# Kernel optimization log

Hardware: AMD Instinct MI355X
Metric: run time of the kernel (lower is better)

The kernel has to match this reference:

```python
import jax, jax.numpy as jnp
import numpy as np

B, T, S, M = 512, 256, 32, 4  # groups, timesteps, state dim, measure dim


def setup_inputs() -> dict:
    key = jax.random.key(0)
    k = jax.random.split(key, 7)
    obs = jax.random.normal(k[0], (B, T, M), jnp.float32)
    # stable transition matrix: scaled orthogonal
    A = jax.random.normal(k[1], (S, S), jnp.float32)
    F = (0.95 * jnp.linalg.qr(A)[0]).astype(jnp.float32)
    # PSD process noise
    Aq = jax.random.normal(k[2], (S, S), jnp.float32)
    Q = (0.05 * (Aq @ Aq.T) / S + 0.01 * jnp.eye(S)).astype(jnp.float32)
    H = (jax.random.normal(k[3], (M, S), jnp.float32) / jnp.sqrt(S)).astype(jnp.float32)
    # PSD measurement noise
    Ar = jax.random.normal(k[4], (M, M), jnp.float32)
    R = ((Ar @ Ar.T) / M + 0.1 * jnp.eye(M)).astype(jnp.float32)
    init_mean = jax.random.normal(k[5], (B, S), jnp.float32)
    Ai = jax.random.normal(k[6], (B, S, S), jnp.float32)
    init_cov = (jnp.einsum('bij,bkj->bik', Ai, Ai) / S + 0.1 * jnp.eye(S)).astype(jnp.float32)
    return {'input': obs, 'F': F, 'Q': Q, 'H': H, 'R': R,
            'init_mean': init_mean, 'init_cov': init_cov}


def reference(input, F, Q, H, R, init_mean, init_cov):
    """One-step-ahead Kalman filter predictions.
    Returns (meas_means [T,B,M], meas_covs [T,B,M,M])."""

    def step(carry, y):
        m, P = carry  # m: [B,S], P: [B,S,S]
        # --- update with observation y (time t-1) ---
        PHt = jnp.einsum('bij,mj->bim', P, H)                    # [B,S,M]
        Smeas = jnp.einsum('ms,bsn->bmn', H, PHt) + R            # [B,M,M]
        # K = P H^T S^{-1}  (S symmetric)
        K = jnp.swapaxes(jnp.linalg.solve(Smeas, jnp.swapaxes(PHt, -1, -2)), -1, -2)  # [B,S,M]
        resid = y - m @ H.T                                      # [B,M]
        m_u = m + jnp.einsum('bsm,bm->bs', K, resid)
        # (I - K H) P ; note H P = PHt^T since P symmetric
        P_u = P - jnp.einsum('bsm,bim->bsi', K, PHt)
        # --- predict ---
        m_p = m_u @ F.T
        P_p = jnp.einsum('ij,bjk,lk->bil', F, P_u, F) + Q
        # --- measurement distribution ---
        mm = m_p @ H.T                                           # [B,M]
        mc = jnp.einsum('ms,bsi,ni->bmn', H, P_p, H) + R         # [B,M,M]
        return (m_p, P_p), (mm, mc)

    # t = 0: measurement of the initial state prediction
    mm0 = init_mean @ H.T
    mc0 = jnp.einsum('ms,bsi,ni->bmn', H, init_cov, H) + R
    obs_tm1 = jnp.swapaxes(input[:, :-1, :], 0, 1)               # [T-1,B,M]
    _, (mms, mcs) = jax.lax.scan(step, (init_mean, init_cov), obs_tm1)
    meas_means = jnp.concatenate([mm0[None], mms], axis=0)       # [T,B,M]
    meas_covs = jnp.concatenate([mc0[None], mcs], axis=0)        # [T,B,M,M]
    return meas_means, meas_covs
```

## Files before the change

kernel.cpp:

```cpp
#include <hip/hip_runtime.h>

#define BB 512
#define TT 256

typedef __attribute__((ext_vector_type(8)))  short bf8;
typedef __attribute__((ext_vector_type(4)))  short bf4;
typedef __attribute__((ext_vector_type(16))) float f16v;
typedef __attribute__((ext_vector_type(4)))  float f4v;

#define MFMA(a,b,c) __builtin_amdgcn_mfma_f32_32x32x16_bf16((a),(b),(c),0,0,0)

static __device__ __forceinline__ unsigned short f2bf_rne(float x) {
    unsigned u = __builtin_bit_cast(unsigned, x);
    return (unsigned short)((u + 0x7FFFu + ((u >> 16) & 1u)) >> 16);
}
static __device__ __forceinline__ float bf2f(unsigned short h) {
    unsigned u = ((unsigned)h) << 16;
    return __builtin_bit_cast(float, u);
}
static __device__ __forceinline__ void tsplit(float x, short& hi, short& lo) {
    unsigned u = __builtin_bit_cast(unsigned, x);
    hi = (short)(u >> 16);
    float hf = __builtin_bit_cast(float, u & 0xFFFF0000u);
    float l  = x - hf;
    lo = (short)(__builtin_bit_cast(unsigned, l) >> 16);
}
static __device__ __forceinline__ bf8 ld8(const unsigned short* p) {
    bf4 a = *(const bf4*)p;
    bf4 b = *(const bf4*)(p + 4);
    bf8 r;
    r[0]=a[0]; r[1]=a[1]; r[2]=a[2]; r[3]=a[3];
    r[4]=b[0]; r[5]=b[1]; r[6]=b[2]; r[7]=b[3];
    return r;
}

__global__ __launch_bounds__(64)
void kalman_v5(const float* __restrict__ obs,
               const float* __restrict__ Fg,
               const float* __restrict__ Qg,
               const float* __restrict__ Hg,
               const float* __restrict__ Rg,
               const float* __restrict__ im,
               const float* __restrict__ ic,
               float* __restrict__ out)
{
    __shared__ __align__(16) unsigned short sT1h[32*36], sT1l[32*36];
    __shared__ __align__(16) unsigned short sPNh[4*36],  sPNl[4*36];
    __shared__ __align__(16) float sFH[36*40];
    __shared__ __align__(16) float sm[32];
    __shared__ __align__(16) float sS[16];
    __shared__ __align__(16) float sRes4[4];

    const int lane = threadIdx.x;
    const int b    = blockIdx.x;
    const int c    = lane & 31;
    const int h    = lane >> 5;

    bf8 Fh[2], Fl[2], Hh[2], Hl[2];
    #pragma unroll
    for (int kk = 0; kk < 2; ++kk) {
        #pragma unroll
        for (int j = 0; j < 8; ++j) {
            int k = kk*16 + h*8 + j;
            float f = Fg[c*32 + k];
            unsigned short fh = f2bf_rne(f);
            Fh[kk][j] = (short)fh;
            Fl[kk][j] = (short)f2bf_rne(f - bf2f(fh));
            float hv = (c < 4) ? Hg[c*32 + k] : 0.f;
            unsigned short hh = f2bf_rne(hv);
            Hh[kk][j] = (short)hh;
            Hl[kk][j] = (short)f2bf_rne(hv - bf2f(hh));
        }
    }

    f16v Qc, P;
    #pragma unroll
    for (int reg = 0; reg < 16; ++reg) {
        int row = (reg & 3) + 8*(reg >> 2) + 4*h;
        Qc[reg] = Qg[row*32 + c];
        P[reg]  = ic[(size_t)b*1024 + row*32 + c];
    }
    float Rc[4] = {0.f, 0.f, 0.f, 0.f};
    if (c < 4) {
        #pragma unroll
        for (int m = 0; m < 4; ++m) Rc[m] = Rg[m*4 + c];
    }

    #pragma unroll
    for (int e = lane; e < 1024; e += 64) sFH[(e >> 5)*40 + (e & 31)] = Fg[e];
    #pragma unroll
    for (int e = lane; e < 128; e += 64) sFH[(32 + (e >> 5))*40 + (e & 31)] = Hg[e];
    if (lane < 32) sm[lane] = im[b*32 + lane];

    const float* dotrow = &sFH[(lane < 32 ? lane : (32 + (lane & 3))) * 40];
    const bool yl = (lane >= 32 && lane < 36);
    const float* obsp = obs + (size_t)b*TT*4 + (yl ? (lane - 32) : 0);
    float* om = out;
    float* oc = out + (size_t)TT * BB * 4;

    float yv = yl ? obsp[0] : 0.f;

    for (int t = 0; t < TT; ++t) {
        float yv_nxt = (yl && t + 1 < TT) ? obsp[(t + 1) * 4] : 0.f;

        float dotv = 0.f;
        #pragma unroll
        for (int q = 0; q < 8; ++q) {
            f4v a = *(const f4v*)&dotrow[4*q];
            f4v mv = *(const f4v*)&sm[4*q];
            dotv += a.x*mv.x + a.y*mv.y + a.z*mv.z + a.w*mv.w;
        }

        float p2[16];
        #pragma unroll
        for (int r = 0; r < 16; ++r) p2[r] = __shfl_xor(P[r], 32, 64);
        float fr[2][8];
        #pragma unroll
        for (int j = 0; j < 4; ++j) {
            fr[0][j]   = h ? p2[4+j]  : P[j];
            fr[0][4+j] = h ? P[4+j]   : p2[j];
            fr[1][j]   = h ? p2[12+j] : P[8+j];
            fr[1][4+j] = h ? P[12+j]  : p2[8+j];
        }
        bf8 Ph[2], Pl[2];
        #pragma unroll
        for (int kk = 0; kk < 2; ++kk)
            #pragma unroll
            for (int j = 0; j < 8; ++j) {
                short hi, lo;
                tsplit(fr[kk][j], hi, lo);
                Ph[kk][j] = hi;
                Pl[kk][j] = lo;
            }

        f16v tA = 0.0f, tB = 0.0f;
        tA = MFMA(Ph[0], Fh[0], tA);  tB = MFMA(Ph[1], Fh[1], tB);
        tA = MFMA(Ph[0], Fl[0], tA);  tB = MFMA(Ph[1], Fl[1], tB);
        tA = MFMA(Pl[0], Fh[0], tA);  tB = MFMA(Pl[1], Fh[1], tB);

        f16v aA = 0.0f, aB = 0.0f;
        aA = MFMA(Hh[0], Ph[0], aA);  aB = MFMA(Hh[1], Ph[1], aB);
        aA = MFMA(Hh[0], Pl[0], aA);  aB = MFMA(Hh[1], Pl[1], aB);
        aA = MFMA(Hl[0], Ph[0], aA);  aB = MFMA(Hl[1], Ph[1], aB);

        if (lane < 32) {
            #pragma unroll
            for (int n = 0; n < 4; ++n) {
                short hi, lo;
                tsplit(aA[n] + aB[n], hi, lo);
                sPNh[n*36 + c] = (unsigned short)hi;
                sPNl[n*36 + c] = (unsigned short)lo;
            }
        }
        {
            f16v Tp = tA + tB;
            #pragma unroll
            for (int q = 0; q < 4; ++q) {
                int r0 = 8*q + 4*h;
                bf4 vh, vl;
                #pragma unroll
                for (int i = 0; i < 4; ++i) {
                    short hi, lo;
                    tsplit(Tp[4*q + i], hi, lo);
                    vh[i] = hi; vl[i] = lo;
                }
                *(bf4*)&sT1h[c*36 + r0] = vh;
                *(bf4*)&sT1l[c*36 + r0] = vl;
            }
        }

        bf8 N0h, N1h, N0l, N1l;
        if (c < 4) {
            N0h = ld8(&sPNh[c*36 + 8*h]);
            N1h = ld8(&sPNh[c*36 + 16 + 8*h]);
            N0l = ld8(&sPNl[c*36 + 8*h]);
            N1l = ld8(&sPNl[c*36 + 16 + 8*h]);
        } else {
            N0h = (bf8)(short)0; N1h = (bf8)(short)0;
            N0l = (bf8)(short)0; N1l = (bf8)(short)0;
        }
        bf8 T0h = ld8(&sT1h[c*36 + 8*h]);
        bf8 T1h_ = ld8(&sT1h[c*36 + 16 + 8*h]);
        bf8 T0l = ld8(&sT1l[c*36 + 8*h]);
        bf8 T1l_ = ld8(&sT1l[c*36 + 16 + 8*h]);

        f16v sA = 0.0f, sB = 0.0f;
        sA = MFMA(Hh[0], N0h, sA);  sB = MFMA(Hh[1], N1h, sB);
        sA = MFMA(Hh[0], N0l, sA);  sB = MFMA(Hh[1], N1l, sB);
        sA = MFMA(Hl[0], N0h, sA);  sB = MFMA(Hl[1], N1h, sB);

        f16v wA = 0.0f, wB = 0.0f;
        wA = MFMA(N0h, Fh[0], wA);  wB = MFMA(N1h, Fh[1], wB);
        wA = MFMA(N0h, Fl[0], wA);  wB = MFMA(N1h, Fl[1], wB);
        wA = MFMA(N0l, Fh[0], wA);  wB = MFMA(N1l, Fh[1], wB);

        f16v zA = Qc, zB = 0.0f;
        zA = MFMA(Fh[0], T0h, zA);  zB = MFMA(Fh[1], T1h_, zB);
        zA = MFMA(Fh[0], T0l, zA);  zB = MFMA(Fh[1], T1l_, zB);
        zA = MFMA(Fl[0], T0h, zA);  zB = MFMA(Fl[1], T1h_, zB);

        float Smr[4];
        #pragma unroll
        for (int m = 0; m < 4; ++m) Smr[m] = sA[m] + sB[m] + Rc[m];
        if (lane < 32 && c < 4) {
            #pragma unroll
            for (int m = 0; m < 4; ++m)
                oc[(((size_t)t*BB + b)*4 + m)*4 + c] = Smr[m];
            *(f4v*)&sS[c*4] = (f4v){Smr[0], Smr[1], Smr[2], Smr[3]};
        }
        if (yl) {
            om[((size_t)t*BB + b)*4 + (lane - 32)] = dotv;
            sRes4[lane - 32] = yv - dotv;
        }

        if (t == TT - 1) break;
        yv = yv_nxt;

        f4v q0 = *(const f4v*)&sS[0];
        f4v q1 = *(const f4v*)&sS[4];
        f4v q2 = *(const f4v*)&sS[8];
        f4v q3 = *(const f4v*)&sS[12];
        const float S0=q0.x,  S1=q1.x,  S2=q2.x,  S3=q3.x;
        const float S4=q0.y,  S5=q1.y,  S6=q2.y,  S7=q3.y;
        const float S8=q0.z,  S9=q1.z,  S10=q2.z, S11=q3.z;
        const float S12=q0.w, S13=q1.w, S14=q2.w, S15=q3.w;

        float nG0, nG1, nG2, nG3, W0, W1, W2, W3;
        {
            const float A2323 = S10*S15 - S11*S14;
            const float A1323 = S9 *S15 - S11*S13;
            const float A1223 = S9 *S14 - S10*S13;
            const float A0323 = S8 *S15 - S11*S12;
            const float A0223 = S8 *S14 - S10*S12;
            const float A0123 = S8 *S13 - S9 *S12;
            const float A2313 = S6 *S15 - S7 *S14;
            const float A1313 = S5 *S15 - S7 *S13;
            const float A1213 = S5 *S14 - S6 *S13;
            const float A2312 = S6 *S11 - S7 *S10;
            const float A1312 = S5 *S11 - S7 *S9;
            const float A1212 = S5 *S10 - S6 *S9;
            const float A0313 = S4 *S15 - S7 *S12;
            const float A0213 = S4 *S14 - S6 *S12;
            const float A0312 = S4 *S11 - S7 *S8;
            const float A0212 = S4 *S10 - S6 *S8;
            const float A0113 = S4 *S13 - S5 *S12;
            const float A0112 = S4 *S9  - S5 *S8;

            const float i00 =  (S5*A2323 - S6*A1323 + S7*A1223);
            const float i10 = -(S4*A2323 - S6*A0323 + S7*A0223);
            const float i20 =  (S4*A1323 - S5*A0323 + S7*A0123);
            const float i30 = -(S4*A1223 - S5*A0223 + S6*A0123);
            const float i01 = -(S1*A2323 - S2*A1323 + S3*A1223);
            const float i11 =  (S0*A2323 - S2*A0323 + S3*A0223);
            const float i21 = -(S0*A1323 - S1*A0323 + S3*A0123);
            const float i31 =  (S0*A1223 - S1*A0223 + S2*A0123);
            const float i02 =  (S1*A2313 - S2*A1313 + S3*A1213);
            const float i12 = -(S0*A2313 - S2*A0313 + S3*A0213);
            const float i22 =  (S0*A1313 - S1*A0313 + S3*A0113);
            const float i32 = -(S0*A1213 - S1*A0213 + S2*A0113);
            const float i03 = -(S1*A2312 - S2*A1312 + S3*A1212);
            const float i13 =  (S0*A2312 - S2*A0312 + S3*A0212);
            const float i23 = -(S0*A1312 - S1*A0312 + S3*A0112);
            const float i33 =  (S0*A1212 - S1*A0212 + S2*A0112);

            const float det = S0*i00 + S1*i10 + S2*i20 + S3*i30;
            const float nid = -1.0f / det;

            W0 = wA[0] + wB[0];
            W1 = wA[1] + wB[1];
            W2 = wA[2] + wB[2];
            W3 = wA[3] + wB[3];

            nG0 = nid * (W0*i00 + W1*i10 + W2*i20 + W3*i30);
            nG1 = nid * (W0*i01 + W1*i11 + W2*i21 + W3*i31);
            nG2 = nid * (W0*i02 + W1*i12 + W2*i22 + W3*i32);
            nG3 = nid * (W0*i03 + W1*i13 + W2*i23 + W3*i33);
        }

        bf8 Gh = (bf8)(short)0, Gl = (bf8)(short)0;
        bf8 Wbh = (bf8)(short)0, Wbl = (bf8)(short)0;
        {
            float ng[4] = {nG0, nG1, nG2, nG3};
            float wv[4] = {W0, W1, W2, W3};
            #pragma unroll
            for (int j2 = 0; j2 < 4; ++j2) {
                short hi, lo;
                tsplit(ng[j2], hi, lo);
                Gh[j2] = hi; Gl[j2] = lo;
                tsplit(wv[j2], hi, lo);
                Wbh[j2] = hi; Wbl[j2] = lo;
            }
        }
        f16v Pn = zA + zB;
        Pn = MFMA(Gh, Wbh, Pn);
        Pn = MFMA(Gh, Wbl, Pn);
        Pn = MFMA(Gl, Wbh, Pn);
        P = Pn;

        {
            f4v rv = *(const f4v*)&sRes4[0];
            if (lane < 32)
                sm[lane] = dotv - (nG0*rv.x + nG1*rv.y + nG2*rv.z + nG3*rv.w);
        }
    }
}

extern "C" void kernel_launch(void* const* d_in, const int* in_sizes, int n_in,
                              void* d_out, int out_size, void* d_ws, size_t ws_size,
                              hipStream_t stream) {
    const float* obs       = (const float*)d_in[0];
    const float* F         = (const float*)d_in[1];
    const float* Q         = (const float*)d_in[2];
    const float* H         = (const float*)d_in[3];
    const float* R         = (const float*)d_in[4];
    const float* init_mean = (const float*)d_in[5];
    const float* init_cov  = (const float*)d_in[6];
    float* out = (float*)d_out;

    kalman_v5<<<BB, 64, 0, stream>>>(obs, F, Q, H, R, init_mean, init_cov, out);
}
```

Baseline: 540.7 us.

## Switch split-precision MFMA from bf16 to fp16 and keep T fragment in registers

Replaces the bf16 hi/lo split MFMAs with fp16 MFMAs, using packed round-toward-zero conversions for the split. The F·P·F^T intermediate is rebuilt with cross-lane shuffles instead of a round trip through LDS. The F/H dot-product row is held in registers rather than read from shared memory, and the Joseph-style gain update is folded into the existing accumulators. These changes cut LDS traffic and conversion cost on the serial per-timestep path, but fp16 has a narrower exponent range than bf16, so values that are very large or very small could lose accuracy.

```diff
diff --git a/kernel.cpp b/kernel.cpp
--- a/kernel.cpp
+++ b/kernel.cpp
@@ -2,40 +2,52 @@
 
 #define BB 512
 #define TT 256
-
-typedef __attribute__((ext_vector_type(8)))  short bf8;
-typedef __attribute__((ext_vector_type(4)))  short bf4;
+#define PS 40
+
+typedef __attribute__((ext_vector_type(2)))  _Float16 h2;
+typedef __attribute__((ext_vector_type(4)))  _Float16 h4;
+typedef __attribute__((ext_vector_type(8)))  _Float16 h8;
+typedef __attribute__((ext_vector_type(4)))  unsigned u4v;
 typedef __attribute__((ext_vector_type(16))) float f16v;
 typedef __attribute__((ext_vector_type(4)))  float f4v;
 
-#define MFMA(a,b,c) __builtin_amdgcn_mfma_f32_32x32x16_bf16((a),(b),(c),0,0,0)
-
-static __device__ __forceinline__ unsigned short f2bf_rne(float x) {
-    unsigned u = __builtin_bit_cast(unsigned, x);
-    return (unsigned short)((u + 0x7FFFu + ((u >> 16) & 1u)) >> 16);
-}
-static __device__ __forceinline__ float bf2f(unsigned short h) {
-    unsigned u = ((unsigned)h) << 16;
-    return __builtin_bit_cast(float, u);
-}
-static __device__ __forceinline__ void tsplit(float x, short& hi, short& lo) {
-    unsigned u = __builtin_bit_cast(unsigned, x);
-    hi = (short)(u >> 16);
-    float hf = __builtin_bit_cast(float, u & 0xFFFF0000u);
-    float l  = x - hf;
-    lo = (short)(__builtin_bit_cast(unsigned, l) >> 16);
-}
-static __device__ __forceinline__ bf8 ld8(const unsigned short* p) {
-    bf4 a = *(const bf4*)p;
-    bf4 b = *(const bf4*)(p + 4);
-    bf8 r;
+#define MFMA(a,b,c) __builtin_amdgcn_mfma_f32_32x32x16_f16((a),(b),(c),0,0,0)
+
+static __device__ __forceinline__ void pksplit(float x0, float x1, unsigned& hi, unsigned& lo) {
+    h2 h = __builtin_bit_cast(h2, __builtin_amdgcn_cvt_pkrtz(x0, x1));
+    h2 l = __builtin_bit_cast(h2, __builtin_amdgcn_cvt_pkrtz(x0 - (float)h[0], x1 - (float)h[1]));
+    hi = __builtin_bit_cast(unsigned, h);
+    lo = __builtin_bit_cast(unsigned, l);
+}
+
+static __device__ __forceinline__ void mkfrag(const f16v M, int h, h8 Ah[2], h8 Al[2]) {
+    unsigned ph[8], pl[8], xh[8], xl[8];
+    #pragma unroll
+    for (int q = 0; q < 8; ++q) pksplit(M[2*q], M[2*q+1], ph[q], pl[q]);
+    #pragma unroll
+    for (int q = 0; q < 8; ++q) {
+        xh[q] = (unsigned)__shfl_xor((int)ph[q], 32, 64);
+        xl[q] = (unsigned)__shfl_xor((int)pl[q], 32, 64);
+    }
+    u4v a0h = { h ? xh[2] : ph[0], h ? xh[3] : ph[1], h ? ph[2] : xh[0], h ? ph[3] : xh[1] };
+    u4v a1h = { h ? xh[6] : ph[4], h ? xh[7] : ph[5], h ? ph[6] : xh[4], h ? ph[7] : xh[5] };
+    u4v a0l = { h ? xl[2] : pl[0], h ? xl[3] : pl[1], h ? pl[2] : xl[0], h ? pl[3] : xl[1] };
+    u4v a1l = { h ? xl[6] : pl[4], h ? xl[7] : pl[5], h ? pl[6] : xl[4], h ? pl[7] : xl[5] };
+    Ah[0] = __builtin_bit_cast(h8, a0h);  Ah[1] = __builtin_bit_cast(h8, a1h);
+    Al[0] = __builtin_bit_cast(h8, a0l);  Al[1] = __builtin_bit_cast(h8, a1l);
+}
+
+static __device__ __forceinline__ h8 ld8h(const _Float16* p) {
+    h4 a = *(const h4*)p;
+    h4 b = *(const h4*)(p + 4);
+    h8 r;
     r[0]=a[0]; r[1]=a[1]; r[2]=a[2]; r[3]=a[3];
     r[4]=b[0]; r[5]=b[1]; r[6]=b[2]; r[7]=b[3];
     return r;
 }
 
-__global__ __launch_bounds__(64)
-void kalman_v5(const float* __restrict__ obs,
+__global__ __launch_bounds__(64, 1)
+void kalman_v7(const float* __restrict__ obs,
                const float* __restrict__ Fg,
                const float* __restrict__ Qg,
                const float* __restrict__ Hg,
@@ -44,9 +56,7 @@
                const float* __restrict__ ic,
                float* __restrict__ out)
 {
-    __shared__ __align__(16) unsigned short sT1h[32*36], sT1l[32*36];
-    __shared__ __align__(16) unsigned short sPNh[4*36],  sPNl[4*36];
-    __shared__ __align__(16) float sFH[36*40];
+    __shared__ __align__(16) _Float16 sPNh[4*PS], sPNl[4*PS];
     __shared__ __align__(16) float sm[32];
     __shared__ __align__(16) float sS[16];
     __shared__ __align__(16) float sRes4[4];
@@ -56,22 +66,27 @@
     const int c    = lane & 31;
     const int h    = lane >> 5;
 
-    bf8 Fh[2], Fl[2], Hh[2], Hl[2];
+    h8 Fh[2], Fl[2], Hh[2], Hl[2];
     #pragma unroll
     for (int kk = 0; kk < 2; ++kk) {
         #pragma unroll
         for (int j = 0; j < 8; ++j) {
             int k = kk*16 + h*8 + j;
             float f = Fg[c*32 + k];
-            unsigned short fh = f2bf_rne(f);
-            Fh[kk][j] = (short)fh;
-            Fl[kk][j] = (short)f2bf_rne(f - bf2f(fh));
+            _Float16 fh = (_Float16)f;
+            Fh[kk][j] = fh;
+            Fl[kk][j] = (_Float16)(f - (float)fh);
             float hv = (c < 4) ? Hg[c*32 + k] : 0.f;
-            unsigned short hh = f2bf_rne(hv);
-            Hh[kk][j] = (short)hh;
-            Hl[kk][j] = (short)f2bf_rne(hv - bf2f(hh));
-        }
-    }
+            _Float16 hh = (_Float16)hv;
+            Hh[kk][j] = hh;
+            Hl[kk][j] = (_Float16)(hv - (float)hh);
+        }
+    }
+
+    float Frow[32];
+    #pragma unroll
+    for (int k = 0; k < 32; ++k)
+        Frow[k] = (lane < 32) ? Fg[c*32 + k] : Hg[(lane & 3)*32 + k];
 
     f16v Qc, P;
     #pragma unroll
@@ -85,14 +100,8 @@
         #pragma unroll
         for (int m = 0; m < 4; ++m) Rc[m] = Rg[m*4 + c];
     }
-
-    #pragma unroll
-    for (int e = lane; e < 1024; e += 64) sFH[(e >> 5)*40 + (e & 31)] = Fg[e];
-    #pragma unroll
-    for (int e = lane; e < 128; e += 64) sFH[(32 + (e >> 5))*40 + (e & 31)] = Hg[e];
     if (lane < 32) sm[lane] = im[b*32 + lane];
 
-    const float* dotrow = &sFH[(lane < 32 ? lane : (32 + (lane & 3))) * 40];
     const bool yl = (lane >= 32 && lane < 36);
     const float* obsp = obs + (size_t)b*TT*4 + (yl ? (lane - 32) : 0);
     float* om = out;
@@ -106,83 +115,46 @@
         float dotv = 0.f;
         #pragma unroll
         for (int q = 0; q < 8; ++q) {
-            f4v a = *(const f4v*)&dotrow[4*q];
             f4v mv = *(const f4v*)&sm[4*q];
-            dotv += a.x*mv.x + a.y*mv.y + a.z*mv.z + a.w*mv.w;
-        }
-
-        float p2[16];
-        #pragma unroll
-        for (int r = 0; r < 16; ++r) p2[r] = __shfl_xor(P[r], 32, 64);
-        float fr[2][8];
-        #pragma unroll
-        for (int j = 0; j < 4; ++j) {
-            fr[0][j]   = h ? p2[4+j]  : P[j];
-            fr[0][4+j] = h ? P[4+j]   : p2[j];
-            fr[1][j]   = h ? p2[12+j] : P[8+j];
-            fr[1][4+j] = h ? P[12+j]  : p2[8+j];
-        }
-        bf8 Ph[2], Pl[2];
-        #pragma unroll
-        for (int kk = 0; kk < 2; ++kk)
-            #pragma unroll
-            for (int j = 0; j < 8; ++j) {
-                short hi, lo;
-                tsplit(fr[kk][j], hi, lo);
-                Ph[kk][j] = hi;
-                Pl[kk][j] = lo;
-            }
+            dotv += Frow[4*q+0]*mv.x + Frow[4*q+1]*mv.y
+                  + Frow[4*q+2]*mv.z + Frow[4*q+3]*mv.w;
+        }
+
+        h8 Ph[2], Pl[2];
+        mkfrag(P, h, Ph, Pl);
+
+        f16v aA = 0.0f, aB = 0.0f;
+        aA = MFMA(Hh[0], Ph[0], aA);  aB = MFMA(Hh[1], Ph[1], aB);
+        aA = MFMA(Hh[0], Pl[0], aA);  aB = MFMA(Hh[1], Pl[1], aB);
+        aA = MFMA(Hl[0], Ph[0], aA);  aB = MFMA(Hl[1], Ph[1], aB);
+
+        if (lane < 32) {
+            unsigned h01, l01, h23, l23;
+            pksplit(aA[0]+aB[0], aA[1]+aB[1], h01, l01);
+            pksplit(aA[2]+aB[2], aA[3]+aB[3], h23, l23);
+            h2 H01 = __builtin_bit_cast(h2, h01), L01 = __builtin_bit_cast(h2, l01);
+            h2 H23 = __builtin_bit_cast(h2, h23), L23 = __builtin_bit_cast(h2, l23);
+            sPNh[0*PS + c] = H01[0];  sPNh[1*PS + c] = H01[1];
+            sPNh[2*PS + c] = H23[0];  sPNh[3*PS + c] = H23[1];
+            sPNl[0*PS + c] = L01[0];  sPNl[1*PS + c] = L01[1];
+            sPNl[2*PS + c] = L23[0];  sPNl[3*PS + c] = L23[1];
+        }
 
         f16v tA = 0.0f, tB = 0.0f;
         tA = MFMA(Ph[0], Fh[0], tA);  tB = MFMA(Ph[1], Fh[1], tB);
         tA = MFMA(Ph[0], Fl[0], tA);  tB = MFMA(Ph[1], Fl[1], tB);
         tA = MFMA(Pl[0], Fh[0], tA);  tB = MFMA(Pl[1], Fh[1], tB);
 
-        f16v aA = 0.0f, aB = 0.0f;
-        aA = MFMA(Hh[0], Ph[0], aA);  aB = MFMA(Hh[1], Ph[1], aB);
-        aA = MFMA(Hh[0], Pl[0], aA);  aB = MFMA(Hh[1], Pl[1], aB);
-        aA = MFMA(Hl[0], Ph[0], aA);  aB = MFMA(Hl[1], Ph[1], aB);
-
-        if (lane < 32) {
-            #pragma unroll
-            for (int n = 0; n < 4; ++n) {
-                short hi, lo;
-                tsplit(aA[n] + aB[n], hi, lo);
-                sPNh[n*36 + c] = (unsigned short)hi;
-                sPNl[n*36 + c] = (unsigned short)lo;
-            }
-        }
-        {
-            f16v Tp = tA + tB;
-            #pragma unroll
-            for (int q = 0; q < 4; ++q) {
-                int r0 = 8*q + 4*h;
-                bf4 vh, vl;
-                #pragma unroll
-                for (int i = 0; i < 4; ++i) {
-                    short hi, lo;
-                    tsplit(Tp[4*q + i], hi, lo);
-                    vh[i] = hi; vl[i] = lo;
-                }
-                *(bf4*)&sT1h[c*36 + r0] = vh;
-                *(bf4*)&sT1l[c*36 + r0] = vl;
-            }
-        }
-
-        bf8 N0h, N1h, N0l, N1l;
+        h8 N0h, N1h, N0l, N1l;
         if (c < 4) {
-            N0h = ld8(&sPNh[c*36 + 8*h]);
-            N1h = ld8(&sPNh[c*36 + 16 + 8*h]);
-            N0l = ld8(&sPNl[c*36 + 8*h]);
-            N1l = ld8(&sPNl[c*36 + 16 + 8*h]);
+            N0h = ld8h(&sPNh[c*PS + 8*h]);
+            N1h = ld8h(&sPNh[c*PS + 16 + 8*h]);
+            N0l = ld8h(&sPNl[c*PS + 8*h]);
+            N1l = ld8h(&sPNl[c*PS + 16 + 8*h]);
         } else {
-            N0h = (bf8)(short)0; N1h = (bf8)(short)0;
-            N0l = (bf8)(short)0; N1l = (bf8)(short)0;
-        }
-        bf8 T0h = ld8(&sT1h[c*36 + 8*h]);
-        bf8 T1h_ = ld8(&sT1h[c*36 + 16 + 8*h]);
-        bf8 T0l = ld8(&sT1l[c*36 + 8*h]);
-        bf8 T1l_ = ld8(&sT1l[c*36 + 16 + 8*h]);
+            N0h = (h8)(_Float16)0; N1h = (h8)(_Float16)0;
+            N0l = (h8)(_Float16)0; N1l = (h8)(_Float16)0;
+        }
 
         f16v sA = 0.0f, sB = 0.0f;
         sA = MFMA(Hh[0], N0h, sA);  sB = MFMA(Hh[1], N1h, sB);
@@ -194,10 +166,14 @@
         wA = MFMA(N0h, Fl[0], wA);  wB = MFMA(N1h, Fl[1], wB);
         wA = MFMA(N0l, Fh[0], wA);  wB = MFMA(N1l, Fh[1], wB);
 
+        f16v Tp = tA + tB;
+        h8 Th[2], Tl[2];
+        mkfrag(Tp, h, Th, Tl);
+
         f16v zA = Qc, zB = 0.0f;
-        zA = MFMA(Fh[0], T0h, zA);  zB = MFMA(Fh[1], T1h_, zB);
-        zA = MFMA(Fh[0], T0l, zA);  zB = MFMA(Fh[1], T1l_, zB);
-        zA = MFMA(Fl[0], T0h, zA);  zB = MFMA(Fl[1], T1h_, zB);
+        zA = MFMA(Fh[0], Th[0], zA);  zB = MFMA(Fh[1], Th[1], zB);
+        zA = MFMA(Fh[0], Tl[0], zA);  zB = MFMA(Fh[1], Tl[1], zB);
+        zA = MFMA(Fl[0], Th[0], zA);  zB = MFMA(Fl[1], Th[1], zB);
 
         float Smr[4];
         #pragma unroll
@@ -277,25 +253,22 @@
             nG3 = nid * (W0*i03 + W1*i13 + W2*i23 + W3*i33);
         }
 
-        bf8 Gh = (bf8)(short)0, Gl = (bf8)(short)0;
-        bf8 Wbh = (bf8)(short)0, Wbl = (bf8)(short)0;
+        h8 Gh8, Gl8, Wh8, Wl8;
         {
-            float ng[4] = {nG0, nG1, nG2, nG3};
-            float wv[4] = {W0, W1, W2, W3};
-            #pragma unroll
-            for (int j2 = 0; j2 < 4; ++j2) {
-                short hi, lo;
-                tsplit(ng[j2], hi, lo);
-                Gh[j2] = hi; Gl[j2] = lo;
-                tsplit(wv[j2], hi, lo);
-                Wbh[j2] = hi; Wbl[j2] = lo;
-            }
-        }
-        f16v Pn = zA + zB;
-        Pn = MFMA(Gh, Wbh, Pn);
-        Pn = MFMA(Gh, Wbl, Pn);
-        Pn = MFMA(Gl, Wbh, Pn);
-        P = Pn;
+            unsigned g01, gl01, g23, gl23, w01, wl01, w23, wl23;
+            pksplit(nG0, nG1, g01, gl01);
+            pksplit(nG2, nG3, g23, gl23);
+            pksplit(W0, W1, w01, wl01);
+            pksplit(W2, W3, w23, wl23);
+            u4v gh = {g01, g23, 0u, 0u}, gl = {gl01, gl23, 0u, 0u};
+            u4v wh = {w01, w23, 0u, 0u}, wl = {wl01, wl23, 0u, 0u};
+            Gh8 = __builtin_bit_cast(h8, gh);  Gl8 = __builtin_bit_cast(h8, gl);
+            Wh8 = __builtin_bit_cast(h8, wh);  Wl8 = __builtin_bit_cast(h8, wl);
+        }
+        zA = MFMA(Gh8, Wh8, zA);
+        zB = MFMA(Gh8, Wl8, zB);
+        zA = MFMA(Gl8, Wh8, zA);
+        P = zA + zB;
 
         {
             f4v rv = *(const f4v*)&sRes4[0];
@@ -317,5 +290,5 @@
     const float* init_cov  = (const float*)d_in[6];
     float* out = (float*)d_out;
 
-    kalman_v5<<<BB, 64, 0, stream>>>(obs, F, Q, H, R, init_mean, init_cov, out);
-}
+    kalman_v7<<<BB, 64, 0, stream>>>(obs, F, Q, H, R, init_mean, init_cov, out);
+}
```

Result: slower. 563.3 us (+4.2%).
